# Kernel tuning notes

Hardware: AMD Instinct MI355X
Metric: run time of the kernel (lower is better)

## Reference

```python
import jax, jax.numpy as jnp
import numpy as np

B, S, H, NH = 8, 4096, 1024, 16
D = H // NH  # head dim = 64


def setup_inputs() -> dict:
    key = jax.random.key(0)
    k1, k2, k3, k4, k5 = jax.random.split(key, 5)
    hidden_states = jax.random.normal(k1, (B, S, H), dtype=jnp.float32)
    attention_mask = jnp.zeros((B, 1, 1, S), dtype=jnp.float32)
    # Linear params (torch convention: y = x @ W.T + b)
    Wq = jax.random.normal(k2, (H, H), dtype=jnp.float32) * 0.02
    bq = jnp.zeros((H,), dtype=jnp.float32)
    Wkv = jax.random.normal(k3, (H, H), dtype=jnp.float32) * 0.02
    bkv = jnp.zeros((H,), dtype=jnp.float32)
    return {"hidden_states": hidden_states, "attention_mask": attention_mask,
            "Wq": Wq, "bq": bq, "Wkv": Wkv, "bkv": bkv}


def reference(hidden_states, attention_mask, Wq, bq, Wkv, bkv):
    scale = 1.0 / jnp.sqrt(jnp.asarray(D, hidden_states.dtype))
    # projections; K and V share the same key_value projection
    q = hidden_states @ Wq.T + bq            # [B,S,H]
    kv = hidden_states @ Wkv.T + bkv         # [B,S,H]
    q = q.reshape(B, S, NH, D).transpose(0, 2, 1, 3)    # [B,h,S,d]
    k = kv.reshape(B, S, NH, D).transpose(0, 2, 1, 3)   # [B,h,S,d] (also V)

    # global token (position 0) attends to all positions
    gq = q[:, :, 0:1, :]                                 # [B,h,1,d]
    g_scores = jnp.einsum('bhqd,bhkd->bhqk', gq, k) * scale + attention_mask
    g_attn = jax.nn.softmax(g_scores, axis=-1)           # [B,h,1,S]
    g_vec = jnp.einsum('bhqk,bhkd->bhqd', g_attn, k)     # [B,h,1,d]

    # local tokens: each attends over 2 keys = {its own key, global vector}
    lq = q[:, :, 1:, :]                                  # [B,h,S-1,d]
    lk = k[:, :, 1:, :]                                  # [B,h,S-1,d]
    s_self = jnp.sum(lq * lk, axis=-1) * scale           # [B,h,S-1]
    s_glob = jnp.sum(lq * g_vec, axis=-1) * scale        # [B,h,S-1] (g_vec broadcasts)
    l_scores = jnp.stack([s_self, s_glob], axis=-1)      # [B,h,S-1,2]
    l_attn = jax.nn.softmax(l_scores, axis=-1)           # [B,h,S-1,2]
    l_vec = l_attn[..., 0:1] * lk + l_attn[..., 1:2] * g_vec  # [B,h,S-1,d]

    ctx = jnp.concatenate([g_vec, l_vec], axis=2)        # [B,h,S,d]
    ctx = ctx.transpose(0, 2, 1, 3).reshape(B, S, H)     # [B,S,H]
    local_attentions = l_attn[:, :, :, None, :]          # [B,h,S-1,1,2] as in torch
    return ctx, local_attentions
```

## Files before the change

### kernel.cpp

```cpp
#include <hip/hip_runtime.h>
#include <hip/hip_bf16.h>
#include <stdint.h>

#define NB 8
#define NS 4096
#define NHID 1024
#define NHEAD 16
#define ND 64
#define NCH 16
#define CHUNK 256

typedef __attribute__((ext_vector_type(8))) __bf16 bf16x8;
typedef __attribute__((ext_vector_type(4))) __bf16 bf16x4;
typedef __attribute__((ext_vector_type(4))) float floatx4;

__device__ __forceinline__ void async_copy16(const __bf16* g, __bf16* l) {
  __builtin_amdgcn_global_load_lds(
      (const __attribute__((address_space(1))) void*)g,
      (__attribute__((address_space(3))) void*)l,
      16, 0, 0);
}

__global__ void cast_f32_to_bf16(const float* __restrict__ in,
                                 __bf16* __restrict__ out, int n) {
  int i = (blockIdx.x * blockDim.x + threadIdx.x) * 4;
  int stride = gridDim.x * blockDim.x * 4;
  for (; i < n; i += stride) {
    float4 v = *(const float4*)(in + i);
    bf16x4 o;
    o[0] = (__bf16)v.x; o[1] = (__bf16)v.y; o[2] = (__bf16)v.z; o[3] = (__bf16)v.w;
    *(bf16x4*)(out + i) = o;
  }
}

__global__ __launch_bounds__(256) void gemm_qkv(
    const __bf16* __restrict__ A,
    const __bf16* __restrict__ W,
    const float* __restrict__ bq, const float* __restrict__ bkv,
    __bf16* __restrict__ Q, __bf16* __restrict__ KV) {
  __shared__ __align__(16) __bf16 As[128 * 64];
  __shared__ __align__(16) __bf16 Bs[128 * 64];
  const int tid  = threadIdx.x;
  const int lane = tid & 63;
  const int wid  = tid >> 6;
  const int tn = blockIdx.x & 15;
  const int tm = blockIdx.x >> 4;
  const int rowBase = tm * 128;
  const int colBase = tn * 128;
  const int wm = wid >> 1, wn = wid & 1;

  floatx4 acc[4][4];
#pragma unroll
  for (int m = 0; m < 4; m++)
#pragma unroll
    for (int n = 0; n < 4; n++)
#pragma unroll
      for (int j = 0; j < 4; j++) acc[m][n][j] = 0.f;

  const int lrow = lane >> 3;
  const int lk   = (lane & 7) * 8;

  for (int kt = 0; kt < 1024; kt += 64) {
#pragma unroll
    for (int i = 0; i < 4; ++i) {
      const int chunk = wid * 4 + i;
      const int r = chunk * 8 + lrow;
      async_copy16(A + (size_t)(rowBase + r) * 1024 + kt + lk, &As[chunk * 512]);
      async_copy16(W + (size_t)(colBase + r) * 1024 + kt + lk, &Bs[chunk * 512]);
    }
    __syncthreads();
#pragma unroll
    for (int ks = 0; ks < 64; ks += 32) {
      bf16x8 af[4], bfr[4];
#pragma unroll
      for (int m = 0; m < 4; m++)
        af[m] = *(const bf16x8*)&As[(wm * 64 + m * 16 + (lane & 15)) * 64 + ks + (lane >> 4) * 8];
#pragma unroll
      for (int n = 0; n < 4; n++)
        bfr[n] = *(const bf16x8*)&Bs[(wn * 64 + n * 16 + (lane & 15)) * 64 + ks + (lane >> 4) * 8];
#pragma unroll
      for (int m = 0; m < 4; m++)
#pragma unroll
        for (int n = 0; n < 4; n++)
          acc[m][n] = __builtin_amdgcn_mfma_f32_16x16x32_bf16(af[m], bfr[n], acc[m][n], 0, 0, 0);
    }
    __syncthreads();
  }
  const int crow0 = (lane >> 4) * 4;
  const int ccol  = lane & 15;
#pragma unroll
  for (int m = 0; m < 4; m++) {
#pragma unroll
    for (int n = 0; n < 4; n++) {
      const int col = colBase + wn * 64 + n * 16 + ccol;
      const float bias = (col < 1024) ? bq[col] : bkv[col - 1024];
#pragma unroll
      for (int j = 0; j < 4; j++) {
        const int row = rowBase + wm * 64 + m * 16 + crow0 + j;
        const float v = acc[m][n][j] + bias;
        if (col < 1024) Q[(size_t)row * 1024 + col] = (__bf16)v;
        else            KV[(size_t)row * 1024 + (col - 1024)] = (__bf16)v;
      }
    }
  }
}

__global__ __launch_bounds__(256) void global_attn_p1(
    const __bf16* __restrict__ Q, const __bf16* __restrict__ KV,
    const float* __restrict__ mask,
    float* __restrict__ pm, float* __restrict__ ps, float* __restrict__ pv) {
  __shared__ float gq[64];
  __shared__ float sc[CHUNK];
  __shared__ float red[256];
  const int bid = blockIdx.x;
  const int c = bid & (NCH - 1);
  const int h = (bid >> 4) & 15;
  const int b = bid >> 8;
  const int tid = threadIdx.x;
  const float scale = 0.125f;

  if (tid < 64) gq[tid] = (float)Q[(size_t)(b * NS) * NHID + h * 64 + tid];
  __syncthreads();

  const int s = c * CHUNK + tid;
  const __bf16* kr = KV + (size_t)(b * NS + s) * NHID + h * 64;
  float dot = 0.f;
#pragma unroll
  for (int d0 = 0; d0 < 64; d0 += 8) {
    bf16x8 kv8 = *(const bf16x8*)(kr + d0);
#pragma unroll
    for (int j = 0; j < 8; j++) dot += gq[d0 + j] * (float)kv8[j];
  }
  const float score = dot * scale + mask[b * NS + s];

  red[tid] = score; __syncthreads();
#pragma unroll
  for (int off = 128; off > 0; off >>= 1) {
    if (tid < off) red[tid] = fmaxf(red[tid], red[tid + off]);
    __syncthreads();
  }
  const float mc = red[0]; __syncthreads();

  const float p = __expf(score - mc);
  sc[tid] = p;
  red[tid] = p; __syncthreads();
#pragma unroll
  for (int off = 128; off > 0; off >>= 1) {
    if (tid < off) red[tid] += red[tid + off];
    __syncthreads();
  }
  const float sumc = red[0]; __syncthreads();

  const int d = tid & 63;
  const int g = tid >> 6;
  const __bf16* kcol = KV + (size_t)(b * NS + c * CHUNK + g * 64) * NHID + h * 64 + d;
  float acc = 0.f;
#pragma unroll 8
  for (int r = 0; r < 64; r++)
    acc += sc[g * 64 + r] * (float)kcol[(size_t)r * NHID];
  red[tid] = acc; __syncthreads();
  if (tid < 64) {
    pv[(size_t)bid * 64 + tid] = red[tid] + red[tid + 64] + red[tid + 128] + red[tid + 192];
    if (tid == 0) { pm[bid] = mc; ps[bid] = sumc; }
  }
}

__global__ __launch_bounds__(64) void global_attn_p2(
    const float* __restrict__ pm, const float* __restrict__ ps,
    const float* __restrict__ pv,
    float* __restrict__ gvec, float* __restrict__ ctx) {
  const int bh = blockIdx.x;
  const int lane = threadIdx.x;
  const int base = bh * NCH;
  float M = -1e30f;
#pragma unroll
  for (int c = 0; c < NCH; c++) M = fmaxf(M, pm[base + c]);
  float tot = 0.f, vec = 0.f;
#pragma unroll
  for (int c = 0; c < NCH; c++) {
    const float w = __expf(pm[base + c] - M);
    tot += ps[base + c] * w;
    vec += pv[(size_t)(base + c) * 64 + lane] * w;
  }
  const float gout = vec / tot;
  const int b = bh >> 4, h = bh & 15;
  gvec[bh * 64 + lane] = gout;
  ctx[(size_t)(b * NS) * NHID + h * 64 + lane] = gout;
}

__global__ __launch_bounds__(256) void local_attn(
    const __bf16* __restrict__ Q, const __bf16* __restrict__ KV,
    const float* __restrict__ gvec, float* __restrict__ ctx,
    float* __restrict__ lattn) {
  __shared__ float gs[NHEAD * 64];
  const int bb = blockIdx.x >> 10;
  const int s0 = (blockIdx.x & 1023) * 4;
  const int tid = threadIdx.x;
  for (int i = tid; i < NHEAD * 64; i += 256) gs[i] = gvec[bb * NHEAD * 64 + i];
  __syncthreads();
  const int wid = tid >> 6, lane = tid & 63;
  const int s = s0 + wid;
  if (s == 0) return;
  const int head = lane >> 2;
  const int dp = (lane & 3) * 16;
  const size_t rowoff = (size_t)(bb * NS + s) * NHID;
  const __bf16* qr = Q + rowoff + head * 64 + dp;
  const __bf16* kr = KV + rowoff + head * 64 + dp;
  float qv[16], kvv[16], gv[16];
  bf16x8 q0 = *(const bf16x8*)qr, q1 = *(const bf16x8*)(qr + 8);
  bf16x8 k0 = *(const bf16x8*)kr, k1 = *(const bf16x8*)(kr + 8);
#pragma unroll
  for (int j = 0; j < 8; j++) {
    qv[j] = (float)q0[j]; qv[j + 8] = (float)q1[j];
    kvv[j] = (float)k0[j]; kvv[j + 8] = (float)k1[j];
  }
#pragma unroll
  for (int j = 0; j < 16; j++) gv[j] = gs[head * 64 + dp + j];
  float sself = 0.f, sglob = 0.f;
#pragma unroll
  for (int j = 0; j < 16; j++) { sself += qv[j] * kvv[j]; sglob += qv[j] * gv[j]; }
  sself += __shfl_xor(sself, 1); sself += __shfl_xor(sself, 2);
  sglob += __shfl_xor(sglob, 1); sglob += __shfl_xor(sglob, 2);
  const float scale = 0.125f;
  sself *= scale; sglob *= scale;
  const float mm = fmaxf(sself, sglob);
  float p0 = __expf(sself - mm), p1 = __expf(sglob - mm);
  const float inv = 1.f / (p0 + p1);
  p0 *= inv; p1 *= inv;
  float* crow = ctx + rowoff + head * 64 + dp;
#pragma unroll
  for (int j4 = 0; j4 < 4; j4++) {
    float4 o;
    o.x = p0 * kvv[j4 * 4 + 0] + p1 * gv[j4 * 4 + 0];
    o.y = p0 * kvv[j4 * 4 + 1] + p1 * gv[j4 * 4 + 1];
    o.z = p0 * kvv[j4 * 4 + 2] + p1 * gv[j4 * 4 + 2];
    o.w = p0 * kvv[j4 * 4 + 3] + p1 * gv[j4 * 4 + 3];
    *(float4*)(crow + j4 * 4) = o;
  }
  if ((lane & 3) == 0) {
    const size_t li = ((size_t)(bb * NHEAD + head) * (NS - 1) + (s - 1)) * 2;
    lattn[li] = p0; lattn[li + 1] = p1;
  }
}

extern "C" void kernel_launch(void* const* d_in, const int* in_sizes, int n_in,
                              void* d_out, int out_size, void* d_ws, size_t ws_size,
                              hipStream_t stream) {
  const float* hs   = (const float*)d_in[0];
  const float* mask = (const float*)d_in[1];
  const float* Wq   = (const float*)d_in[2];
  const float* bq   = (const float*)d_in[3];
  const float* Wkv  = (const float*)d_in[4];
  const float* bkv  = (const float*)d_in[5];
  float* ctx   = (float*)d_out;
  float* lattn = ctx + (size_t)NB * NS * NHID;

  __bf16* hsb = (__bf16*)d_ws;
  __bf16* Wb  = hsb + (size_t)33554432;
  __bf16* Qb  = Wb  + (size_t)2097152;
  __bf16* KVb = Qb  + (size_t)33554432;
  float*  gvec = (float*)(KVb + (size_t)33554432);
  float*  pm   = gvec + 8192;
  float*  ps   = pm + 2048;
  float*  pv   = ps + 2048;

  cast_f32_to_bf16<<<4096, 256, 0, stream>>>(hs, hsb, 33554432);
  cast_f32_to_bf16<<<512, 256, 0, stream>>>(Wq, Wb, 1048576);
  cast_f32_to_bf16<<<512, 256, 0, stream>>>(Wkv, Wb + (size_t)1048576, 1048576);
  gemm_qkv<<<4096, 256, 0, stream>>>(hsb, Wb, bq, bkv, Qb, KVb);
  global_attn_p1<<<NB * NHEAD * NCH, 256, 0, stream>>>(Qb, KVb, mask, pm, ps, pv);
  global_attn_p2<<<NB * NHEAD, 64, 0, stream>>>(pm, ps, pv, gvec, ctx);
  local_attn<<<NB * (NS / 4), 256, 0, stream>>>(Qb, KVb, gvec, ctx, lattn);
}
```

Measured before the change: 531.7 us.

## Rewrite QKV GEMM with 256x256 tiles and a double-buffered swizzled LDS pipeline

Rewrites the QKV projection GEMM around 256x256 output tiles with 8 waves of 512 threads, so each loaded operand is reused across more MFMAs. Operand tiles are staged into a double-buffered, XOR-swizzled 128KB LDS region with async global-to-LDS copies, and loads for the next K-steps are issued while the current step computes. Manual vmcnt waits and raw barriers sequence this, and MFMA blocks run at raised wave priority. Block indices are also remapped for L2 locality. In exchange there is more register pressure from 8x4 accumulators, a single block per CU because of the LDS footprint, and fragile hand-counted wait logic.

```diff
diff --git a/kernel.cpp b/kernel.cpp
--- a/kernel.cpp
+++ b/kernel.cpp
@@ -9,6 +9,7 @@
 #define ND 64
 #define NCH 16
 #define CHUNK 256
+#define NT 16
 
 typedef __attribute__((ext_vector_type(8))) __bf16 bf16x8;
 typedef __attribute__((ext_vector_type(4))) __bf16 bf16x4;
@@ -33,73 +34,133 @@
   }
 }
 
-__global__ __launch_bounds__(256) void gemm_qkv(
+
+__device__ __forceinline__ void stage_half(const __bf16* __restrict__ G, int rb,
+                                           int T, int kh, int matB,
+                                           char* smem, int tid, int wid) {
+  const uint32_t regionOff = (matB ? 65536u : 0u) + (uint32_t)(T & 1) * 32768u
+                           + (uint32_t)kh * 16384u;
+#pragma unroll
+  for (int j = 0; j < 2; ++j) {
+    uint32_t P = (uint32_t)(j * 512 + tid) * 16u;
+    uint32_t L = P ^ (((P >> 7) & 3u) << 4);
+    uint32_t r = L >> 6;
+    uint32_t c = (L >> 4) & 3u;
+    const __bf16* src = G + (size_t)(rb + (int)r) * 1024 + T * 64 + kh * 32 + (int)c * 8;
+    async_copy16(src, (__bf16*)(smem + regionOff + (uint32_t)j * 8192u
+                                + (uint32_t)wid * 1024u));
+  }
+}
+
+__device__ __forceinline__ bf16x8 lds_frag(const char* smem, uint32_t base,
+                                           int kk, int row, int hi4) {
+  uint32_t Lrel = (uint32_t)kk * 16384u + (uint32_t)row * 64u + (uint32_t)hi4 * 16u;
+  uint32_t phys = Lrel ^ (((Lrel >> 7) & 3u) << 4);
+  return *(const bf16x8*)(smem + base + phys);
+}
+
+#define BARRIER asm volatile("s_barrier" ::: "memory")
+#define WAIT_LGKM0 asm volatile("s_waitcnt lgkmcnt(0)" ::: "memory")
+#define VM8 asm volatile("s_waitcnt vmcnt(8)" ::: "memory")
+#define VM4 asm volatile("s_waitcnt vmcnt(4)" ::: "memory")
+#define VM0 asm volatile("s_waitcnt vmcnt(0)" ::: "memory")
+
+#define PHASE(KK, FMB, READB, STAGE_STMT, DRAIN_STMT)                          \
+  do {                                                                         \
+    if (READB) {                                                               \
+      _Pragma("unroll")                                                        \
+      for (int fn = 0; fn < 4; ++fn)                                           \
+        bfrag[fn] = lds_frag(smem, 65536u + sl, KK, wn * 64 + fn * 16 + l15, hi4); \
+    }                                                                          \
+    _Pragma("unroll")                                                          \
+    for (int fi = 0; fi < 4; ++fi)                                             \
+      afrag[fi] = lds_frag(smem, sl, KK, wm * 128 + (FMB + fi) * 16 + l15, hi4); \
+    STAGE_STMT;                                                                \
+    BARRIER;                                                                   \
+    WAIT_LGKM0;                                                                \
+    __builtin_amdgcn_s_setprio(1);                                             \
+    _Pragma("unroll")                                                          \
+    for (int fi = 0; fi < 4; ++fi) {                                           \
+      _Pragma("unroll")                                                        \
+      for (int fn = 0; fn < 4; ++fn)                                           \
+        acc[FMB + fi][fn] = __builtin_amdgcn_mfma_f32_16x16x32_bf16(           \
+            afrag[fi], bfrag[fn], acc[FMB + fi][fn], 0, 0, 0);                 \
+    }                                                                          \
+    __builtin_amdgcn_s_setprio(0);                                             \
+    DRAIN_STMT;                                                                \
+    BARRIER;                                                                   \
+  } while (0)
+
+__global__ __launch_bounds__(512, 2) void gemm_qkv(
     const __bf16* __restrict__ A,
     const __bf16* __restrict__ W,
     const float* __restrict__ bq, const float* __restrict__ bkv,
     __bf16* __restrict__ Q, __bf16* __restrict__ KV) {
-  __shared__ __align__(16) __bf16 As[128 * 64];
-  __shared__ __align__(16) __bf16 Bs[128 * 64];
-  const int tid  = threadIdx.x;
+  __shared__ __align__(1024) char smem[131072];
+  const int tid = threadIdx.x;
   const int lane = tid & 63;
-  const int wid  = tid >> 6;
-  const int tn = blockIdx.x & 15;
-  const int tm = blockIdx.x >> 4;
-  const int rowBase = tm * 128;
-  const int colBase = tn * 128;
-  const int wm = wid >> 1, wn = wid & 1;
-
-  floatx4 acc[4][4];
-#pragma unroll
-  for (int m = 0; m < 4; m++)
+  const int wid = tid >> 6;
+  const int wm = wid >> 2;
+  const int wn = wid & 3;
+  const int l15 = lane & 15;
+  const int hi4 = lane >> 4;
+
+  const int bid = blockIdx.x;
+  const int swz = ((bid & 7) << 7) | (bid >> 3);
+  const int tn = swz & 7;
+  const int tm = swz >> 3;
+  const int rowBase = tm * 256;
+  const int colBase = tn * 256;
+
+  floatx4 acc[8][4];
+#pragma unroll
+  for (int m = 0; m < 8; m++)
 #pragma unroll
     for (int n = 0; n < 4; n++)
 #pragma unroll
       for (int j = 0; j < 4; j++) acc[m][n][j] = 0.f;
 
-  const int lrow = lane >> 3;
-  const int lk   = (lane & 7) * 8;
-
-  for (int kt = 0; kt < 1024; kt += 64) {
-#pragma unroll
-    for (int i = 0; i < 4; ++i) {
-      const int chunk = wid * 4 + i;
-      const int r = chunk * 8 + lrow;
-      async_copy16(A + (size_t)(rowBase + r) * 1024 + kt + lk, &As[chunk * 512]);
-      async_copy16(W + (size_t)(colBase + r) * 1024 + kt + lk, &Bs[chunk * 512]);
-    }
-    __syncthreads();
-#pragma unroll
-    for (int ks = 0; ks < 64; ks += 32) {
-      bf16x8 af[4], bfr[4];
-#pragma unroll
-      for (int m = 0; m < 4; m++)
-        af[m] = *(const bf16x8*)&As[(wm * 64 + m * 16 + (lane & 15)) * 64 + ks + (lane >> 4) * 8];
-#pragma unroll
-      for (int n = 0; n < 4; n++)
-        bfr[n] = *(const bf16x8*)&Bs[(wn * 64 + n * 16 + (lane & 15)) * 64 + ks + (lane >> 4) * 8];
-#pragma unroll
-      for (int m = 0; m < 4; m++)
-#pragma unroll
-        for (int n = 0; n < 4; n++)
-          acc[m][n] = __builtin_amdgcn_mfma_f32_16x16x32_bf16(af[m], bfr[n], acc[m][n], 0, 0, 0);
-    }
-    __syncthreads();
-  }
-  const int crow0 = (lane >> 4) * 4;
-  const int ccol  = lane & 15;
-#pragma unroll
-  for (int m = 0; m < 4; m++) {
-#pragma unroll
-    for (int n = 0; n < 4; n++) {
-      const int col = colBase + wn * 64 + n * 16 + ccol;
-      const float bias = (col < 1024) ? bq[col] : bkv[col - 1024];
+  stage_half(A, rowBase, 0, 0, 0, smem, tid, wid);
+  stage_half(W, colBase, 0, 0, 1, smem, tid, wid);
+  stage_half(A, rowBase, 0, 1, 0, smem, tid, wid);
+  stage_half(W, colBase, 0, 1, 1, smem, tid, wid);
+  stage_half(A, rowBase, 1, 0, 0, smem, tid, wid);
+  stage_half(W, colBase, 1, 0, 1, smem, tid, wid);
+  VM4;
+  BARRIER;
+
+  bf16x8 afrag[4], bfrag[4];
+#pragma unroll 1
+  for (int t = 0; t < NT; ++t) {
+    const uint32_t sl = (uint32_t)(t & 1) * 32768u;
+    PHASE(0, 0, 1,
+          { if (t + 1 < NT) stage_half(A, rowBase, t + 1, 1, 0, smem, tid, wid); },
+          ;);
+    PHASE(0, 4, 0,
+          { if (t + 1 < NT) stage_half(W, colBase, t + 1, 1, 1, smem, tid, wid); },
+          { if (t < NT - 1) { VM8; } else { VM0; } });
+    PHASE(1, 0, 1,
+          { if (t + 2 < NT) stage_half(A, rowBase, t + 2, 0, 0, smem, tid, wid); },
+          ;);
+    PHASE(1, 4, 0,
+          { if (t + 2 < NT) stage_half(W, colBase, t + 2, 0, 1, smem, tid, wid); },
+          { if (t < NT - 2) { VM8; } else if (t == NT - 2) { VM4; } });
+  }
+
+  const bool isQ = (colBase < 1024);
+  __bf16* __restrict__ dst = isQ ? Q : KV;
+  const float* __restrict__ bias = isQ ? bq : bkv;
+  const int colOff = isQ ? colBase : (colBase - 1024);
+#pragma unroll
+  for (int fm = 0; fm < 8; fm++) {
+#pragma unroll
+    for (int fn = 0; fn < 4; fn++) {
+      const int col = colOff + wn * 64 + fn * 16 + l15;
+      const float bv = bias[col];
 #pragma unroll
       for (int j = 0; j < 4; j++) {
-        const int row = rowBase + wm * 64 + m * 16 + crow0 + j;
-        const float v = acc[m][n][j] + bias;
-        if (col < 1024) Q[(size_t)row * 1024 + col] = (__bf16)v;
-        else            KV[(size_t)row * 1024 + (col - 1024)] = (__bf16)v;
+        const int row = rowBase + wm * 128 + fm * 16 + hi4 * 4 + j;
+        dst[(size_t)row * 1024 + col] = (__bf16)(acc[fm][fn][j] + bv);
       }
     }
   }
@@ -267,7 +328,7 @@
   cast_f32_to_bf16<<<4096, 256, 0, stream>>>(hs, hsb, 33554432);
   cast_f32_to_bf16<<<512, 256, 0, stream>>>(Wq, Wb, 1048576);
   cast_f32_to_bf16<<<512, 256, 0, stream>>>(Wkv, Wb + (size_t)1048576, 1048576);
-  gemm_qkv<<<4096, 256, 0, stream>>>(hsb, Wb, bq, bkv, Qb, KVb);
+  gemm_qkv<<<1024, 512, 0, stream>>>(hsb, Wb, bq, bkv, Qb, KVb);
   global_attn_p1<<<NB * NHEAD * NCH, 256, 0, stream>>>(Qb, KVb, mask, pm, ps, pv);
   global_attn_p2<<<NB * NHEAD, 64, 0, stream>>>(pm, ps, pv, gvec, ctx);
   local_attn<<<NB * (NS / 4), 256, 0, stream>>>(Qb, KVb, gvec, ctx, lattn);
```

After: 461.4 us. -13.2%, faster.
